# Optimization experiments

Hardware: AMD Instinct MI355X
Metric: run time of the kernel (lower is better)

Reference implementation:

```python
import jax, jax.numpy as jnp
import numpy as np

M = 1024       # number of retained frequency bins (init kwarg m)
LMBDA = 0.1    # regularizer (init kwarg lmbda)


def _next_pow2(n):
    return 1 << int(np.ceil(np.log2(n)))


def _single_fv(ts, m):
    # ts: [b, L, d] real. Zero-pad time to next pow2, FFT along time, keep first m bins.
    b, L, d = ts.shape
    Lp = _next_pow2(L)
    x = jnp.pad(ts, ((0, 0), (0, Lp - L), (0, 0))).transpose(0, 2, 1)  # [b, d, Lp]
    Q = jnp.fft.fft(x.astype(jnp.complex64), axis=-1)                   # unnormalized FFT (matches legacy torch.fft)
    return Q[:, :, :m]                                                   # [b, d, m] complex


def setup_inputs() -> dict:
    key = jax.random.key(0)
    k1, k2, k3 = jax.random.split(key, 3)
    B, L, D = 16, 4096, 512
    max_len = 4096
    return {
        "ts_a": jax.random.normal(k1, (B, L, D), dtype=jnp.float32),
        "ts_b": jax.random.normal(k2, (B, L, D), dtype=jnp.float32),
        "offsets": jax.random.normal(k3, (B, 2 * max_len), dtype=jnp.float32),
    }


def reference(ts_a, ts_b, offsets):
    m, lmbda = M, LMBDA
    Qa = _single_fv(ts_a, m)            # [b, d, m]
    Qb = _single_fv(ts_b, m)
    max_len = offsets.shape[-1] // 2    # merge() re-derives max_len from offsets
    Lp2 = _next_pow2(max_len)

    def corr(Q, B_):
        # regularized circulant cross-correlation in the Fourier domain
        den = jnp.sum(Q.real * Q.real + Q.imag * Q.imag, axis=1, keepdims=True) + lmbda  # [b,1,m]
        S = jnp.sum(jnp.conj(Q) * B_, axis=1, keepdims=True) / den                       # [b,1,m]
        S = jnp.pad(S, ((0, 0), (0, 0), (0, Lp2 - m)))                                   # pad freq bins
        R = jnp.fft.ifft(S, axis=-1).real                                                # normalized IFFT (matches torch.ifft)
        return R[:, 0, :max_len]                                                          # [b, max_len]

    Rab = corr(Qa, Qb)
    Rba = corr(Qb, Qa)
    return jnp.concatenate([Rab[:, ::-1], Rba], axis=1)  # first half flipped, as in torch code
```

## Files before the change

### kernel.cpp

```cpp
#include <hip/hip_runtime.h>

#define NB 16
#define LT 4096
#define ND 512
#define MBINS 1024
#define LMBDA 0.1f
#define DLB 8
#define FWD_THREADS 1024

__device__ __forceinline__ float2 cmulf(float2 a, float2 b) {
    return make_float2(a.x * b.x - a.y * b.y, a.x * b.y + a.y * b.x);
}
__device__ __forceinline__ float2 caddf(float2 a, float2 b) { return make_float2(a.x + b.x, a.y + b.y); }
__device__ __forceinline__ float2 csubf(float2 a, float2 b) { return make_float2(a.x - b.x, a.y - b.y); }

__device__ __forceinline__ int rev4_10(int k) {
    unsigned r = __brev((unsigned)k) >> 22;
    return (int)(((r & 0x155u) << 1) | ((r >> 1) & 0x155u));
}
__device__ __forceinline__ int rev4_12(int t) {
    unsigned r = __brev((unsigned)t) >> 20;
    return (int)(((r & 0x555u) << 1) | ((r >> 1) & 0x555u));
}


__global__ __launch_bounds__(FWD_THREADS)
void cte_fwd_kernel(const float* __restrict__ A, const float* __restrict__ Bp,
                    float* __restrict__ ws) {
    __shared__ float2 z[8192];
    __shared__ float2 tw[256];

    const int tid = threadIdx.x;
    const int logical = (blockIdx.x & 7) * (gridDim.x >> 3) + (blockIdx.x >> 3);
    const int bb    = logical >> 6;
    const int chunk = logical & 63;
    const int d0    = chunk * DLB;

    if (tid < 256) {
        float s, c;
        sincosf(-6.283185307179586f * (float)tid * (1.0f / 1024.0f), &s, &c);
        tw[tid] = make_float2(c, s);
    }

    const int dl  = tid & 7;
    const int g   = tid >> 3;
    const int dp  = tid & 3;
    const int t1l = tid >> 2;

    float2 X1[8], Z4[8];
#pragma unroll
    for (int j = 0; j < 8; ++j) {
        X1[j] = make_float2(0.f, 0.f);
        Z4[j] = make_float2(0.f, 0.f);
    }

    for (int t2 = 0; t2 < 4; ++t2) {
        __syncthreads();

        float2 A4[4], B4[4];
#pragma unroll
        for (int it = 0; it < 4; ++it) {
            size_t off = ((size_t)(bb * LT + 4 * (t1l + 256 * it) + t2)) * ND + d0 + 2 * dp;
            A4[it] = *(const float2*)(A + off);
            B4[it] = *(const float2*)(Bp + off);
        }
        {
            float2 w1 = tw[t1l];
            float2 w2 = cmulf(w1, w1);
            float2 w3 = cmulf(w2, w1);
#pragma unroll
            for (int c = 0; c < 2; ++c) {
                float2 x0 = c ? make_float2(A4[0].y, B4[0].y) : make_float2(A4[0].x, B4[0].x);
                float2 x1 = c ? make_float2(A4[1].y, B4[1].y) : make_float2(A4[1].x, B4[1].x);
                float2 x2 = c ? make_float2(A4[2].y, B4[2].y) : make_float2(A4[2].x, B4[2].x);
                float2 x3 = c ? make_float2(A4[3].y, B4[3].y) : make_float2(A4[3].x, B4[3].x);
                float2 t0  = caddf(x0, x2), t1v = csubf(x0, x2);
                float2 t2v = caddf(x1, x3), t3  = csubf(x1, x3);
                float2 y0 = caddf(t0, t2v);
                float2 y2 = cmulf(csubf(t0, t2v), w2);
                float2 y1 = cmulf(make_float2(t1v.x + t3.y, t1v.y - t3.x), w1);
                float2 y3 = cmulf(make_float2(t1v.x - t3.y, t1v.y + t3.x), w3);
                int ix = (t1l << 3) + 2 * dp + c;
                z[ix]        = y0;
                z[ix + 2048] = y1;
                z[ix + 4096] = y2;
                z[ix + 6144] = y3;
            }
        }
        __syncthreads();

#pragma unroll
        for (int st = 0; st < 4; ++st) {
            const int lgm  = 6 - 2 * st;
            const int m    = 1 << lgm;
            const int step = 256 >> lgm;
#pragma unroll
            for (int r2 = 0; r2 < 2; ++r2) {
                int u   = r2 * FWD_THREADS + tid;
                int dli = u & 7;
                int bf  = u >> 3;
                int j   = bf & (m - 1);
                int i0  = ((bf >> lgm) << (lgm + 2)) + j;
                int ix  = (i0 << 3) + dli;
                float2 a0 = z[ix];
                float2 a1 = z[ix + 8 * m];
                float2 a2 = z[ix + 16 * m];
                float2 a3 = z[ix + 24 * m];
                float2 t0  = caddf(a0, a2), t1v = csubf(a0, a2);
                float2 t2v = caddf(a1, a3), t3  = csubf(a1, a3);
                float2 w1 = tw[j * step];
                float2 w2 = cmulf(w1, w1);
                float2 w3 = cmulf(w2, w1);
                z[ix]          = caddf(t0, t2v);
                z[ix + 8 * m]  = cmulf(make_float2(t1v.x + t3.y, t1v.y - t3.x), w1);
                z[ix + 16 * m] = cmulf(csubf(t0, t2v), w2);
                z[ix + 24 * m] = cmulf(make_float2(t1v.x - t3.y, t1v.y + t3.x), w3);
            }
            __syncthreads();
        }

        float2 w, wstep;
        {
            float s, c;
            sincosf(-1.5339807878856412e-03f * (float)(t2 * g), &s, &c);
            w = make_float2(c, s);
            sincosf(-1.9634954084936207e-01f * (float)t2, &s, &c);
            wstep = make_float2(c, s);
        }
#pragma unroll
        for (int j = 0; j < 8; ++j) {
            int k   = g + 128 * j;
            int rk  = rev4_10(k);
            int k2  = (1024 - k) & 1023;
            int rk2 = rev4_10(k2);
            float2 Ya = z[(rk << 3) + dl];
            float2 Yb = z[(rk2 << 3) + dl];
            X1[j].x += w.x * Ya.x - w.y * Ya.y;
            X1[j].y += w.x * Ya.y + w.y * Ya.x;
            Z4[j].x += w.x * Yb.x + w.y * Yb.y;
            Z4[j].y += w.x * Yb.y - w.y * Yb.x;
            w = cmulf(w, wstep);
        }
    }

#pragma unroll
    for (int j = 0; j < 8; ++j) {
        int k = g + 128 * j;
        float Ar = 0.5f * (X1[j].x + Z4[j].x);
        float Ai = 0.5f * (X1[j].y - Z4[j].y);
        float Br = 0.5f * (X1[j].y + Z4[j].y);
        float Bi = 0.5f * (Z4[j].x - X1[j].x);
        float da = Ar * Ar + Ai * Ai;
        float db = Br * Br + Bi * Bi;
        float cr = Ar * Br + Ai * Bi;
        float ci = Ar * Bi - Ai * Br;
        for (int msk = 1; msk < DLB; msk <<= 1) {
            da += __shfl_xor(da, msk);
            db += __shfl_xor(db, msk);
            cr += __shfl_xor(cr, msk);
            ci += __shfl_xor(ci, msk);
        }
        if (dl == 0) {
            atomicAdd(&ws[0 * NB * MBINS + bb * MBINS + k], da);
            atomicAdd(&ws[1 * NB * MBINS + bb * MBINS + k], db);
            atomicAdd(&ws[2 * NB * MBINS + bb * MBINS + k], cr);
            atomicAdd(&ws[3 * NB * MBINS + bb * MBINS + k], ci);
        }
    }
}

__global__ __launch_bounds__(512)
void cte_inv_kernel(const float* __restrict__ ws, float* __restrict__ out) {
    __shared__ float2 zz[4096];
    __shared__ float2 tw[1024];
    const int tid = threadIdx.x;
    const int bb  = blockIdx.x >> 1;
    const int dir = blockIdx.x & 1;

    for (int i = tid; i < 1024; i += 512) {
        float s, c;
        sincosf(6.283185307179586f * (float)i * (1.0f / 4096.0f), &s, &c);
        tw[i] = make_float2(c, s);
    }
    for (int i = tid; i < 4096; i += 512) {
        float2 v = make_float2(0.f, 0.f);
        if (i < MBINS) {
            float den = ws[(dir ? 1 : 0) * NB * MBINS + bb * MBINS + i] + LMBDA;
            float cr  = ws[2 * NB * MBINS + bb * MBINS + i];
            float ci  = ws[3 * NB * MBINS + bb * MBINS + i];
            if (dir) ci = -ci;
            v = make_float2(cr / den, ci / den);
        }
        zz[i] = v;
    }
    __syncthreads();

#pragma unroll
    for (int st = 0; st < 6; ++st) {
        const int lgm  = 10 - 2 * st;
        const int m    = 1 << lgm;
        const int step = 1024 >> lgm;
#pragma unroll
        for (int r = 0; r < 2; ++r) {
            int bf = r * 512 + tid;
            int j  = bf & (m - 1);
            int i0 = ((bf >> lgm) << (lgm + 2)) + j;
            float2 a0 = zz[i0], a1 = zz[i0 + m], a2 = zz[i0 + 2 * m], a3 = zz[i0 + 3 * m];
            float2 t0  = caddf(a0, a2), t1v = csubf(a0, a2);
            float2 t2v = caddf(a1, a3), t3  = csubf(a1, a3);
            float2 y0 = caddf(t0, t2v);
            float2 y2 = csubf(t0, t2v);
            float2 y1 = make_float2(t1v.x - t3.y, t1v.y + t3.x);
            float2 y3 = make_float2(t1v.x + t3.y, t1v.y - t3.x);
            if (m > 1) {
                float2 w1 = tw[j * step];
                float2 w2 = cmulf(w1, w1);
                float2 w3 = cmulf(w2, w1);
                y1 = cmulf(y1, w1);
                y2 = cmulf(y2, w2);
                y3 = cmulf(y3, w3);
            }
            zz[i0] = y0; zz[i0 + m] = y1; zz[i0 + 2 * m] = y2; zz[i0 + 3 * m] = y3;
        }
        __syncthreads();
    }

    const float scale = 1.0f / 4096.0f;
    for (int t = tid; t < 4096; t += 512) {
        int rt = rev4_12(t);
        float val = zz[rt].x * scale;
        int col = (dir == 0) ? (4095 - t) : (4096 + t);
        out[(size_t)bb * 8192 + col] = val;
    }
}

extern "C" void kernel_launch(void* const* d_in, const int* in_sizes, int n_in,
                              void* d_out, int out_size, void* d_ws, size_t ws_size,
                              hipStream_t stream) {
    const float* a = (const float*)d_in[0];
    const float* b = (const float*)d_in[1];
    float* out = (float*)d_out;
    float* ws  = (float*)d_ws;

    hipMemsetAsync(d_ws, 0, 4 * NB * MBINS * sizeof(float), stream);
    cte_fwd_kernel<<<dim3(NB * (ND / DLB)), dim3(FWD_THREADS), 0, stream>>>(a, b, ws);
    cte_inv_kernel<<<dim3(NB * 2), dim3(512), 0, stream>>>(ws, out);
}
```

Baseline: 193.0 us.

## Restructure forward FFT to two channels per block with full-length radix-4 FFTs

Each block now handles 2 channels instead of 8 and runs two complete 2048-point radix-4 FFTs (even and odd time samples) in shared memory, followed by one radix-2 stage and a final split combine. This replaces the previous four-pass 1024-point FFT plus per-bin twiddle accumulation. A XOR swizzle on shared-memory indices is added to avoid bank conflicts, and the grid grows fourfold. The aim is to cut the redundant accumulation work and the repeated sync passes, at the cost of narrower global loads per row (8 bytes per channel pair) and more blocks issuing atomics.

```diff
diff --git a/kernel.cpp b/kernel.cpp
--- a/kernel.cpp
+++ b/kernel.cpp
@@ -5,7 +5,6 @@
 #define ND 512
 #define MBINS 1024
 #define LMBDA 0.1f
-#define DLB 8
 #define FWD_THREADS 1024
 
 __device__ __forceinline__ float2 cmulf(float2 a, float2 b) {
@@ -14,13 +13,19 @@
 __device__ __forceinline__ float2 caddf(float2 a, float2 b) { return make_float2(a.x + b.x, a.y + b.y); }
 __device__ __forceinline__ float2 csubf(float2 a, float2 b) { return make_float2(a.x - b.x, a.y - b.y); }
 
-__device__ __forceinline__ int rev4_10(int k) {
-    unsigned r = __brev((unsigned)k) >> 22;
-    return (int)(((r & 0x155u) << 1) | ((r >> 1) & 0x155u));
-}
 __device__ __forceinline__ int rev4_12(int t) {
     unsigned r = __brev((unsigned)t) >> 20;
     return (int)(((r & 0x555u) << 1) | ((r >> 1) & 0x555u));
+}
+
+__device__ __forceinline__ int zi(int idx) {
+    int h = (idx >> 6) ^ (idx >> 9);
+    return idx ^ ((h & 7) << 1);
+}
+
+__device__ __forceinline__ int arow(int k) {
+    return ((k & 3) << 9) | (((k >> 2) & 3) << 7) | (((k >> 4) & 3) << 5)
+         | (((k >> 6) & 3) << 3) | (((k >> 8) & 3) << 1) | ((k >> 10) & 1);
 }
 
 
@@ -28,144 +33,139 @@
 void cte_fwd_kernel(const float* __restrict__ A, const float* __restrict__ Bp,
                     float* __restrict__ ws) {
     __shared__ float2 z[8192];
-    __shared__ float2 tw[256];
+    __shared__ float2 tw[512];
 
     const int tid = threadIdx.x;
     const int logical = (blockIdx.x & 7) * (gridDim.x >> 3) + (blockIdx.x >> 3);
-    const int bb    = logical >> 6;
-    const int chunk = logical & 63;
-    const int d0    = chunk * DLB;
-
-    if (tid < 256) {
+    const int bb    = logical >> 8;
+    const int chunk = logical & 255;
+    const int d0    = chunk * 2;
+
+    const int n     = tid & 511;
+    const int which = tid >> 9;
+    float2 A4[4], B4[4];
+#pragma unroll
+    for (int i = 0; i < 4; ++i) {
+        size_t off = ((size_t)(bb * LT + 2 * (n + 512 * i) + which)) * ND + d0;
+        A4[i] = *(const float2*)(A + off);
+        B4[i] = *(const float2*)(Bp + off);
+    }
+
+    if (tid < 512) {
         float s, c;
-        sincosf(-6.283185307179586f * (float)tid * (1.0f / 1024.0f), &s, &c);
+        sincosf(-6.283185307179586f * (float)tid * (1.0f / 2048.0f), &s, &c);
         tw[tid] = make_float2(c, s);
     }
-
-    const int dl  = tid & 7;
-    const int g   = tid >> 3;
-    const int dp  = tid & 3;
-    const int t1l = tid >> 2;
-
-    float2 X1[8], Z4[8];
-#pragma unroll
-    for (int j = 0; j < 8; ++j) {
-        X1[j] = make_float2(0.f, 0.f);
-        Z4[j] = make_float2(0.f, 0.f);
-    }
-
-    for (int t2 = 0; t2 < 4; ++t2) {
-        __syncthreads();
-
-        float2 A4[4], B4[4];
-#pragma unroll
-        for (int it = 0; it < 4; ++it) {
-            size_t off = ((size_t)(bb * LT + 4 * (t1l + 256 * it) + t2)) * ND + d0 + 2 * dp;
-            A4[it] = *(const float2*)(A + off);
-            B4[it] = *(const float2*)(Bp + off);
-        }
-        {
-            float2 w1 = tw[t1l];
+    __syncthreads();
+
+    {
+        float2 w1 = tw[n];
+        float2 w2 = cmulf(w1, w1);
+        float2 w3 = cmulf(w2, w1);
+        const int base = which * 4096;
+#pragma unroll
+        for (int c = 0; c < 2; ++c) {
+            float2 x0 = c ? make_float2(A4[0].y, B4[0].y) : make_float2(A4[0].x, B4[0].x);
+            float2 x1 = c ? make_float2(A4[1].y, B4[1].y) : make_float2(A4[1].x, B4[1].x);
+            float2 x2 = c ? make_float2(A4[2].y, B4[2].y) : make_float2(A4[2].x, B4[2].x);
+            float2 x3 = c ? make_float2(A4[3].y, B4[3].y) : make_float2(A4[3].x, B4[3].x);
+            float2 t0  = caddf(x0, x2), t1v = csubf(x0, x2);
+            float2 t2v = caddf(x1, x3), t3  = csubf(x1, x3);
+            int ib = base + 2 * n + c;
+            z[zi(ib)]        = caddf(t0, t2v);
+            z[zi(ib + 1024)] = cmulf(make_float2(t1v.x + t3.y, t1v.y - t3.x), w1);
+            z[zi(ib + 2048)] = cmulf(csubf(t0, t2v), w2);
+            z[zi(ib + 3072)] = cmulf(make_float2(t1v.x - t3.y, t1v.y + t3.x), w3);
+        }
+    }
+    __syncthreads();
+
+#pragma unroll
+    for (int st = 0; st < 4; ++st) {
+        const int lgm  = 7 - 2 * st;
+        const int m    = 1 << lgm;
+        const int step = 512 >> lgm;
+#pragma unroll
+        for (int r2 = 0; r2 < 2; ++r2) {
+            int u   = r2 * FWD_THREADS + tid;
+            int c   = u & 1;
+            int bf  = (u >> 1) & 511;
+            int fft = u >> 10;
+            int j   = bf & (m - 1);
+            int i0  = ((bf >> lgm) << (lgm + 2)) + j;
+            int ib  = fft * 4096 + c;
+            int ix0 = zi(ib + 2 * i0);
+            int ix1 = zi(ib + 2 * (i0 + m));
+            int ix2 = zi(ib + 2 * (i0 + 2 * m));
+            int ix3 = zi(ib + 2 * (i0 + 3 * m));
+            float2 a0 = z[ix0], a1 = z[ix1], a2 = z[ix2], a3 = z[ix3];
+            float2 t0  = caddf(a0, a2), t1v = csubf(a0, a2);
+            float2 t2v = caddf(a1, a3), t3  = csubf(a1, a3);
+            float2 w1 = tw[j * step];
             float2 w2 = cmulf(w1, w1);
             float2 w3 = cmulf(w2, w1);
-#pragma unroll
-            for (int c = 0; c < 2; ++c) {
-                float2 x0 = c ? make_float2(A4[0].y, B4[0].y) : make_float2(A4[0].x, B4[0].x);
-                float2 x1 = c ? make_float2(A4[1].y, B4[1].y) : make_float2(A4[1].x, B4[1].x);
-                float2 x2 = c ? make_float2(A4[2].y, B4[2].y) : make_float2(A4[2].x, B4[2].x);
-                float2 x3 = c ? make_float2(A4[3].y, B4[3].y) : make_float2(A4[3].x, B4[3].x);
-                float2 t0  = caddf(x0, x2), t1v = csubf(x0, x2);
-                float2 t2v = caddf(x1, x3), t3  = csubf(x1, x3);
-                float2 y0 = caddf(t0, t2v);
-                float2 y2 = cmulf(csubf(t0, t2v), w2);
-                float2 y1 = cmulf(make_float2(t1v.x + t3.y, t1v.y - t3.x), w1);
-                float2 y3 = cmulf(make_float2(t1v.x - t3.y, t1v.y + t3.x), w3);
-                int ix = (t1l << 3) + 2 * dp + c;
-                z[ix]        = y0;
-                z[ix + 2048] = y1;
-                z[ix + 4096] = y2;
-                z[ix + 6144] = y3;
-            }
+            z[ix0] = caddf(t0, t2v);
+            z[ix1] = cmulf(make_float2(t1v.x + t3.y, t1v.y - t3.x), w1);
+            z[ix2] = cmulf(csubf(t0, t2v), w2);
+            z[ix3] = cmulf(make_float2(t1v.x - t3.y, t1v.y + t3.x), w3);
         }
         __syncthreads();
-
-#pragma unroll
-        for (int st = 0; st < 4; ++st) {
-            const int lgm  = 6 - 2 * st;
-            const int m    = 1 << lgm;
-            const int step = 256 >> lgm;
-#pragma unroll
-            for (int r2 = 0; r2 < 2; ++r2) {
-                int u   = r2 * FWD_THREADS + tid;
-                int dli = u & 7;
-                int bf  = u >> 3;
-                int j   = bf & (m - 1);
-                int i0  = ((bf >> lgm) << (lgm + 2)) + j;
-                int ix  = (i0 << 3) + dli;
-                float2 a0 = z[ix];
-                float2 a1 = z[ix + 8 * m];
-                float2 a2 = z[ix + 16 * m];
-                float2 a3 = z[ix + 24 * m];
-                float2 t0  = caddf(a0, a2), t1v = csubf(a0, a2);
-                float2 t2v = caddf(a1, a3), t3  = csubf(a1, a3);
-                float2 w1 = tw[j * step];
-                float2 w2 = cmulf(w1, w1);
-                float2 w3 = cmulf(w2, w1);
-                z[ix]          = caddf(t0, t2v);
-                z[ix + 8 * m]  = cmulf(make_float2(t1v.x + t3.y, t1v.y - t3.x), w1);
-                z[ix + 16 * m] = cmulf(csubf(t0, t2v), w2);
-                z[ix + 24 * m] = cmulf(make_float2(t1v.x - t3.y, t1v.y + t3.x), w3);
-            }
-            __syncthreads();
-        }
-
-        float2 w, wstep;
-        {
-            float s, c;
-            sincosf(-1.5339807878856412e-03f * (float)(t2 * g), &s, &c);
-            w = make_float2(c, s);
-            sincosf(-1.9634954084936207e-01f * (float)t2, &s, &c);
-            wstep = make_float2(c, s);
-        }
-#pragma unroll
-        for (int j = 0; j < 8; ++j) {
-            int k   = g + 128 * j;
-            int rk  = rev4_10(k);
-            int k2  = (1024 - k) & 1023;
-            int rk2 = rev4_10(k2);
-            float2 Ya = z[(rk << 3) + dl];
-            float2 Yb = z[(rk2 << 3) + dl];
-            X1[j].x += w.x * Ya.x - w.y * Ya.y;
-            X1[j].y += w.x * Ya.y + w.y * Ya.x;
-            Z4[j].x += w.x * Yb.x + w.y * Yb.y;
-            Z4[j].y += w.x * Yb.y - w.y * Yb.x;
-            w = cmulf(w, wstep);
-        }
-    }
-
-#pragma unroll
-    for (int j = 0; j < 8; ++j) {
-        int k = g + 128 * j;
-        float Ar = 0.5f * (X1[j].x + Z4[j].x);
-        float Ai = 0.5f * (X1[j].y - Z4[j].y);
-        float Br = 0.5f * (X1[j].y + Z4[j].y);
-        float Bi = 0.5f * (Z4[j].x - X1[j].x);
+    }
+
+#pragma unroll
+    for (int r2 = 0; r2 < 4; ++r2) {
+        int u   = r2 * FWD_THREADS + tid;
+        int c   = u & 1;
+        int pr  = (u >> 1) & 1023;
+        int fft = u >> 11;
+        int ia  = zi(fft * 4096 + 4 * pr + c);
+        int ib2 = zi(fft * 4096 + 4 * pr + 2 + c);
+        float2 a = z[ia], b = z[ib2];
+        z[ia]  = caddf(a, b);
+        z[ib2] = csubf(a, b);
+    }
+    __syncthreads();
+
+    const int dl = tid & 1;
+    const int g  = tid >> 1;
+    float2 w;
+    {
+        float s, c;
+        sincosf(-1.5339807878856412e-03f * (float)g, &s, &c);
+        w = make_float2(c, s);
+    }
+    const float2 wstep = make_float2(0.707106781186547524f, -0.707106781186547524f);
+#pragma unroll
+    for (int jj = 0; jj < 2; ++jj) {
+        int k  = g + 512 * jj;
+        int mk = (2048 - k) & 2047;
+        int ak = arow(k), am = arow(mk);
+        float2 Ek = z[zi(2 * ak + dl)];
+        float2 Ok = z[zi(4096 + 2 * ak + dl)];
+        float2 Em = z[zi(2 * am + dl)];
+        float2 Om = z[zi(4096 + 2 * am + dl)];
+        float2 X1 = caddf(Ek, cmulf(w, Ok));
+        float2 Z4 = make_float2(Em.x + w.x * Om.x + w.y * Om.y,
+                                Em.y + w.x * Om.y - w.y * Om.x);
+        float Ar = 0.5f * (X1.x + Z4.x);
+        float Ai = 0.5f * (X1.y - Z4.y);
+        float Br = 0.5f * (X1.y + Z4.y);
+        float Bi = 0.5f * (Z4.x - X1.x);
         float da = Ar * Ar + Ai * Ai;
         float db = Br * Br + Bi * Bi;
         float cr = Ar * Br + Ai * Bi;
         float ci = Ar * Bi - Ai * Br;
-        for (int msk = 1; msk < DLB; msk <<= 1) {
-            da += __shfl_xor(da, msk);
-            db += __shfl_xor(db, msk);
-            cr += __shfl_xor(cr, msk);
-            ci += __shfl_xor(ci, msk);
-        }
+        da += __shfl_xor(da, 1);
+        db += __shfl_xor(db, 1);
+        cr += __shfl_xor(cr, 1);
+        ci += __shfl_xor(ci, 1);
         if (dl == 0) {
             atomicAdd(&ws[0 * NB * MBINS + bb * MBINS + k], da);
             atomicAdd(&ws[1 * NB * MBINS + bb * MBINS + k], db);
             atomicAdd(&ws[2 * NB * MBINS + bb * MBINS + k], cr);
             atomicAdd(&ws[3 * NB * MBINS + bb * MBINS + k], ci);
         }
+        w = cmulf(w, wstep);
     }
 }
 
@@ -243,6 +243,6 @@
     float* ws  = (float*)d_ws;
 
     hipMemsetAsync(d_ws, 0, 4 * NB * MBINS * sizeof(float), stream);
-    cte_fwd_kernel<<<dim3(NB * (ND / DLB)), dim3(FWD_THREADS), 0, stream>>>(a, b, ws);
+    cte_fwd_kernel<<<dim3(NB * (ND / 2)), dim3(FWD_THREADS), 0, stream>>>(a, b, ws);
     cte_inv_kernel<<<dim3(NB * 2), dim3(512), 0, stream>>>(ws, out);
 }
```

Result: slower. 210.9 us (+9.2%).

## Fold last radix-4 FFT stage into per-thread bin extraction

Applied to the files above, without the earlier changes.

Drops the fourth shared-memory radix-4 stage and its barrier. Each thread instead performs the final butterflies in registers on four quads and applies twiddles while accumulating bins, so the forward and mirror (N-k) bins come straight from butterfly outputs. This cuts one full LDS read/write pass and one __syncthreads per time-phase. In exchange it adds twiddle recurrences, extra sincosf calls and index logic for picking the mirror bin, with some risk of numerical or indexing mistakes.

```diff
diff --git a/kernel.cpp b/kernel.cpp
--- a/kernel.cpp
+++ b/kernel.cpp
@@ -14,13 +14,25 @@
 __device__ __forceinline__ float2 caddf(float2 a, float2 b) { return make_float2(a.x + b.x, a.y + b.y); }
 __device__ __forceinline__ float2 csubf(float2 a, float2 b) { return make_float2(a.x - b.x, a.y - b.y); }
 
-__device__ __forceinline__ int rev4_10(int k) {
-    unsigned r = __brev((unsigned)k) >> 22;
-    return (int)(((r & 0x155u) << 1) | ((r >> 1) & 0x155u));
+__device__ __forceinline__ int rev4_8(int k) {
+    return ((k & 3) << 6) | ((k & 12) << 2) | ((k >> 2) & 12) | ((k >> 6) & 3);
 }
 __device__ __forceinline__ int rev4_12(int t) {
     unsigned r = __brev((unsigned)t) >> 20;
     return (int)(((r & 0x555u) << 1) | ((r >> 1) & 0x555u));
+}
+
+__device__ __forceinline__ void quad_bfly(const float2* zz, int rbase, int dl, float2 y[4]) {
+    float2 a0 = zz[rbase + dl];
+    float2 a1 = zz[rbase + 8 + dl];
+    float2 a2 = zz[rbase + 16 + dl];
+    float2 a3 = zz[rbase + 24 + dl];
+    float2 t0  = caddf(a0, a2), t1v = csubf(a0, a2);
+    float2 t2v = caddf(a1, a3), t3  = csubf(a1, a3);
+    y[0] = caddf(t0, t2v);
+    y[1] = make_float2(t1v.x + t3.y, t1v.y - t3.x);
+    y[2] = csubf(t0, t2v);
+    y[3] = make_float2(t1v.x - t3.y, t1v.y + t3.x);
 }
 
 
@@ -47,11 +59,17 @@
     const int dp  = tid & 3;
     const int t1l = tid >> 2;
 
-    float2 X1[8], Z4[8];
+    const int g2 = (128 - g) & 127;
+    const int rA = rev4_8(g)        << 5;
+    const int rB = rev4_8(g + 128)  << 5;
+    const int rC = rev4_8(g2)       << 5;
+    const int rD = rev4_8(g2 + 128) << 5;
+
+    float2 X1[8], G[8];
 #pragma unroll
     for (int j = 0; j < 8; ++j) {
         X1[j] = make_float2(0.f, 0.f);
-        Z4[j] = make_float2(0.f, 0.f);
+        G[j]  = make_float2(0.f, 0.f);
     }
 
     for (int t2 = 0; t2 < 4; ++t2) {
@@ -90,7 +108,7 @@
         __syncthreads();
 
 #pragma unroll
-        for (int st = 0; st < 4; ++st) {
+        for (int st = 0; st < 3; ++st) {
             const int lgm  = 6 - 2 * st;
             const int m    = 1 << lgm;
             const int step = 256 >> lgm;
@@ -119,37 +137,73 @@
             __syncthreads();
         }
 
-        float2 w, wstep;
+        float2 wg, w128, w256, vC;
         {
             float s, c;
             sincosf(-1.5339807878856412e-03f * (float)(t2 * g), &s, &c);
-            w = make_float2(c, s);
+            wg = make_float2(c, s);
             sincosf(-1.9634954084936207e-01f * (float)t2, &s, &c);
-            wstep = make_float2(c, s);
-        }
-#pragma unroll
-        for (int j = 0; j < 8; ++j) {
-            int k   = g + 128 * j;
-            int rk  = rev4_10(k);
-            int k2  = (1024 - k) & 1023;
-            int rk2 = rev4_10(k2);
-            float2 Ya = z[(rk << 3) + dl];
-            float2 Yb = z[(rk2 << 3) + dl];
-            X1[j].x += w.x * Ya.x - w.y * Ya.y;
-            X1[j].y += w.x * Ya.y + w.y * Ya.x;
-            Z4[j].x += w.x * Yb.x + w.y * Yb.y;
-            Z4[j].y += w.x * Yb.y - w.y * Yb.x;
-            w = cmulf(w, wstep);
+            w128 = make_float2(c, s);
+            sincosf(-3.9269908169872414e-01f * (float)t2, &s, &c);
+            w256 = make_float2(c, s);
+            sincosf(-1.5339807878856412e-03f * (float)(t2 * g2), &s, &c);
+            float2 tmir = make_float2(c, s);
+            float mix = (t2 & 1) ? 0.f : ((t2 & 2) ? -1.f : 1.f);
+            float miy = (t2 & 1) ? ((t2 & 2) ? -1.f : 1.f) : 0.f;
+            vC = make_float2(mix * tmir.x - miy * tmir.y, mix * tmir.y + miy * tmir.x);
+        }
+        {
+            float2 y[4], wq, p;
+            quad_bfly(z, rA, dl, y);
+            wq = wg;
+#pragma unroll
+            for (int q = 0; q < 4; ++q) {
+                p = cmulf(wq, y[q]);
+                X1[2 * q] = caddf(X1[2 * q], p);
+                wq = cmulf(wq, w256);
+            }
+            quad_bfly(z, rB, dl, y);
+            wq = cmulf(wg, w128);
+#pragma unroll
+            for (int q = 0; q < 4; ++q) {
+                p = cmulf(wq, y[q]);
+                X1[2 * q + 1] = caddf(X1[2 * q + 1], p);
+                wq = cmulf(wq, w256);
+            }
+            quad_bfly(z, rC, dl, y);
+            wq = vC;
+#pragma unroll
+            for (int q = 0; q < 4; ++q) {
+                p = cmulf(wq, y[q]);
+                G[2 * q] = caddf(G[2 * q], p);
+                wq = cmulf(wq, w256);
+            }
+            quad_bfly(z, rD, dl, y);
+            wq = cmulf(vC, w128);
+#pragma unroll
+            for (int q = 0; q < 4; ++q) {
+                p = cmulf(wq, y[q]);
+                G[2 * q + 1] = caddf(G[2 * q + 1], p);
+                wq = cmulf(wq, w256);
+            }
         }
     }
 
 #pragma unroll
     for (int j = 0; j < 8; ++j) {
         int k = g + 128 * j;
-        float Ar = 0.5f * (X1[j].x + Z4[j].x);
-        float Ai = 0.5f * (X1[j].y - Z4[j].y);
-        float Br = 0.5f * (X1[j].y + Z4[j].y);
-        float Bi = 0.5f * (Z4[j].x - X1[j].x);
+        float2 P = X1[j];
+        float2 Xm;
+        if (k == 0) {
+            Xm = P;
+        } else {
+            int j2 = ((1024 - k) - g2) >> 7;
+            Xm = G[j2];
+        }
+        float Ar = 0.5f * (P.x + Xm.x);
+        float Ai = 0.5f * (P.y - Xm.y);
+        float Br = 0.5f * (P.y + Xm.y);
+        float Bi = 0.5f * (Xm.x - P.x);
         float da = Ar * Ar + Ai * Ai;
         float db = Br * Br + Bi * Bi;
         float cr = Ar * Br + Ai * Bi;
```

Result: slower. 287.8 us (+49.1%).
